# Performance work log

Measured on AMD Instinct MI355X. Metric: run time of the kernel, lower is better.

The kernel has to match this reference:

```python
import jax, jax.numpy as jnp
import numpy as np

NUM_CLASSES = 20
N_IN = 1024      # input_capsule_num
C_IN = 128       # in_channels
C_OUT = 64       # out_channels
NUM_ITERS = 3


def squash(x, axis):
    # squash_v1: scale = sqrt(|s|^2) / (0.5 + |s|^2)
    s2 = jnp.sum(x * x, axis=axis, keepdims=True)
    scale = jnp.sqrt(s2) / (0.5 + s2)
    return scale * x


def setup_inputs() -> dict:
    key = jax.random.key(0)
    kx, kw = jax.random.split(key)
    x = jax.random.normal(kx, (32, N_IN, C_IN), dtype=jnp.float32)
    # xavier_uniform over the torch [1, N, C, out, in] tensor: fan_in = in, fan_out = out
    limit = float(np.sqrt(6.0 / (C_IN + C_OUT)))
    w1 = jax.random.uniform(kw, (N_IN, NUM_CLASSES, C_OUT, C_IN), dtype=jnp.float32,
                            minval=-limit, maxval=limit)
    return {"x": x, "w1": w1}


def reference(x, w1):
    # u_hat[b,n,c,d] = w1[n,c,d,i] @ x[b,n,i]  (torch.matmul of [B,N,C,out,in] @ [B,N,C,in,1])
    u_hat = jnp.einsum('ncdi,bni->bncd', w1, x)  # [B, N, C, D]
    B = x.shape[0]
    b_ij = jnp.zeros((B, N_IN, NUM_CLASSES), dtype=u_hat.dtype)
    u_hat_sq = squash(u_hat, axis=3)  # squash over out-channel dim (loop-invariant)
    v = None
    for i in range(NUM_ITERS):
        c = jax.nn.softmax(b_ij, axis=2)                 # softmax over classes
        c = c / jnp.sum(c, axis=1, keepdims=True)        # normalize over input capsules
        s = jnp.einsum('bnc,bncd->bcd', c, u_hat)        # weighted sum over n
        v = squash(s, axis=2)                            # [B, C, D]
        if i < NUM_ITERS - 1:
            dd = 1.0 - jnp.sum((u_hat_sq - v[:, None]) ** 2, axis=3)  # [B, N, C]
            b_ij = b_ij + dd
    poses = v[..., None]                                  # [B, C, D, 1]
    activations = jnp.sqrt(jnp.sum(poses ** 2, axis=2))   # [B, C, 1]
    return poses, activations
```

## Files before the change

kernel.cpp:

```cpp
#include <hip/hip_runtime.h>
#include <hip/hip_bf16.h>


#define NCLS 20
#define NIN  1024
#define CIN  128
#define DOUT 64
#define BATCH 32
#define MCD  1280

typedef __attribute__((ext_vector_type(8))) short bf16x8;
typedef __attribute__((ext_vector_type(4))) float f32x4;

__device__ __forceinline__ float b2f(unsigned short u) {
    union { unsigned int i; float f; } v; v.i = ((unsigned int)u) << 16; return v.f;
}
__device__ __forceinline__ unsigned short f2b_rne(float f) {
    union { float f; unsigned int i; } v; v.f = f;
    unsigned int x = v.i;
    return (unsigned short)((x + 0x7fffu + ((x >> 16) & 1u)) >> 16);
}
__device__ __forceinline__ void cvt_hilo(const float* v, bf16x8& h, bf16x8& l) {
#pragma unroll
    for (int j = 0; j < 8; ++j) {
        unsigned short hb = f2b_rne(v[j]);
        h[j] = (short)hb;
        l[j] = (short)f2b_rne(v[j] - b2f(hb));
    }
}

__global__ __launch_bounds__(256) void pass_uhat(
    const float* __restrict__ x, const float* __restrict__ W,
    unsigned short* __restrict__ uhat)
{
    const int n    = blockIdx.x >> 1;
    const int half = blockIdx.x & 1;
    const int t    = threadIdx.x;
    const int wave = t >> 6;
    const int lane = t & 63;
    const int lm   = lane & 15;
    const int lq   = lane >> 4;

    bf16x8 xh[2][4], xl[2][4];
#pragma unroll
    for (int mt = 0; mt < 2; ++mt) {
        const float* xrow = x + ((size_t)(mt * 16 + lm) * NIN + n) * CIN + lq * 8;
#pragma unroll
        for (int ks = 0; ks < 4; ++ks) {
            float v[8];
            *reinterpret_cast<float4*>(&v[0]) = *reinterpret_cast<const float4*>(xrow + ks * 32);
            *reinterpret_cast<float4*>(&v[4]) = *reinterpret_cast<const float4*>(xrow + ks * 32 + 4);
            cvt_hilo(v, xh[mt][ks], xl[mt][ks]);
        }
    }

    const int nt0 = half * 40 + wave * 10;
    for (int ntc = 0; ntc < 10; ++ntc) {
        const int nt = nt0 + ntc;
        const float* wp = W + ((size_t)n * MCD + nt * 16 + lm) * CIN + lq * 8;
        f32x4 acc0 = {0.f, 0.f, 0.f, 0.f};
        f32x4 acc1 = {0.f, 0.f, 0.f, 0.f};
#pragma unroll
        for (int ks = 0; ks < 4; ++ks) {
            float v[8];
            *reinterpret_cast<float4*>(&v[0]) = *reinterpret_cast<const float4*>(wp + ks * 32);
            *reinterpret_cast<float4*>(&v[4]) = *reinterpret_cast<const float4*>(wp + ks * 32 + 4);
            bf16x8 wh, wl;
            cvt_hilo(v, wh, wl);
            acc0 = __builtin_amdgcn_mfma_f32_16x16x32_bf16(xh[0][ks], wh, acc0, 0, 0, 0);
            acc1 = __builtin_amdgcn_mfma_f32_16x16x32_bf16(xh[1][ks], wh, acc1, 0, 0, 0);
            acc0 = __builtin_amdgcn_mfma_f32_16x16x32_bf16(xh[0][ks], wl, acc0, 0, 0, 0);
            acc1 = __builtin_amdgcn_mfma_f32_16x16x32_bf16(xh[1][ks], wl, acc1, 0, 0, 0);
            acc0 = __builtin_amdgcn_mfma_f32_16x16x32_bf16(xl[0][ks], wh, acc0, 0, 0, 0);
            acc1 = __builtin_amdgcn_mfma_f32_16x16x32_bf16(xl[1][ks], wh, acc1, 0, 0, 0);
        }
        const int cd = nt * 16 + lm;
#pragma unroll
        for (int mt = 0; mt < 2; ++mt) {
            f32x4 a = mt ? acc1 : acc0;
#pragma unroll
            for (int r = 0; r < 4; ++r) {
                int br = mt * 16 + lq * 4 + r;
                uhat[((size_t)br * NIN + n) * MCD + cd] = f2b_rne(a[r]);
            }
        }
    }
}

__global__ __launch_bounds__(320) void pass_s0(
    const unsigned short* __restrict__ uhat, float* __restrict__ s0raw)
{
    const int b     = blockIdx.x >> 4;
    const int chunk = blockIdx.x & 15;
    const int t     = threadIdx.x;

    const ushort4* base = reinterpret_cast<const ushort4*>(
        uhat + ((size_t)b * NIN + chunk * 64) * MCD) + t;
    float a0 = 0.f, a1 = 0.f, a2 = 0.f, a3 = 0.f;
#pragma unroll 4
    for (int k = 0; k < 64; ++k) {
        ushort4 u = base[(size_t)k * 320];
        a0 += b2f(u.x); a1 += b2f(u.y); a2 += b2f(u.z); a3 += b2f(u.w);
    }
    float* dst = s0raw + (size_t)b * MCD + t * 4;
    atomicAdd(dst + 0, a0);
    atomicAdd(dst + 1, a1);
    atomicAdd(dst + 2, a2);
    atomicAdd(dst + 3, a3);
}

__global__ void pass_v(const float* __restrict__ sraw, const float* __restrict__ Zc,
                       float invz_uniform, float* __restrict__ vbuf,
                       float* __restrict__ vn2,
                       float* __restrict__ out_poses, float* __restrict__ out_act)
{
    const int bc   = blockIdx.x;
    const int lane = threadIdx.x;
    const int idx  = bc * 64 + lane;
    float inv = (Zc != nullptr) ? (1.0f / Zc[bc]) : invz_uniform;
    float s  = sraw[idx] * inv;
    float s2 = s * s;
#pragma unroll
    for (int o = 32; o >= 1; o >>= 1) s2 += __shfl_xor(s2, o, 64);
    float norm  = sqrtf(s2);
    float scale = norm / (0.5f + s2);
    float v = scale * s;
    vbuf[idx] = v;
    float vn = scale * scale * s2;
    if (lane == 0) vn2[bc] = vn;
    if (out_poses != nullptr) {
        out_poses[idx] = v;
        if (lane == 0) out_act[bc] = sqrtf(vn);
    }
}

__global__ __launch_bounds__(256) void pass_route(
    const unsigned short* __restrict__ uhat, const float* __restrict__ vbuf,
    const float* __restrict__ vn2, float* __restrict__ bij,
    float* __restrict__ snext, float* __restrict__ Znext)
{
    const int b     = blockIdx.x >> 5;
    const int chunk = blockIdx.x & 31;
    const int t     = threadIdx.x;
    const int wave  = t >> 6;
    const int lane  = t & 63;

    __shared__ float Vs[20 * 65];
    __shared__ float sred[4][20 * 65];
    __shared__ float qrow[4][20], prow[4][20], scrow[4][20], zred[4][20];

    for (int idx = t; idx < 20 * 65; idx += 256) {
        int cc = idx / 65, dd = idx % 65;
        Vs[idx] = (dd < 64) ? vbuf[(size_t)b * MCD + cc * 64 + dd] : 0.f;
    }
    __syncthreads();

    const int cmy   = lane >> 4;
    const int dbase = (lane & 15) * 4;
    const float vnb = vn2[b * NCLS + (lane < 20 ? lane : 0)];

    float sacc[5][4];
#pragma unroll
    for (int tt = 0; tt < 5; ++tt)
#pragma unroll
        for (int j = 0; j < 4; ++j) sacc[tt][j] = 0.f;
    float zacc = 0.f;

    for (int k = 0; k < 8; ++k) {
        const int n = chunk * 32 + wave * 8 + k;
        const ushort4* up = reinterpret_cast<const ushort4*>(
            uhat + ((size_t)b * NIN + n) * MCD);

        float uf[5][4];
#pragma unroll
        for (int tt = 0; tt < 5; ++tt) {
            ushort4 uq = up[tt * 64 + lane];
            uf[tt][0] = b2f(uq.x); uf[tt][1] = b2f(uq.y);
            uf[tt][2] = b2f(uq.z); uf[tt][3] = b2f(uq.w);
        }
#pragma unroll
        for (int tt = 0; tt < 5; ++tt) {
            int cc = tt * 4 + cmy;
            float q = 0.f, p = 0.f;
#pragma unroll
            for (int j = 0; j < 4; ++j) {
                float u = uf[tt][j];
                q = fmaf(u, u, q);
                p = fmaf(u, Vs[cc * 65 + dbase + j], p);
            }
#pragma unroll
            for (int o = 8; o >= 1; o >>= 1) {
                q += __shfl_xor(q, o, 16);
                p += __shfl_xor(p, o, 16);
            }
            if ((lane & 15) == 0) { qrow[wave][cc] = q; prow[wave][cc] = p; }
        }
        {
            float val = -1e30f;
            if (lane < 20) {
                float q  = qrow[wave][lane];
                float p  = prow[wave][lane];
                float qs = sqrtf(q);
                float su = qs / (0.5f + q);
                float dd = 1.f - su * su * q + 2.f * su * p - vnb;
                size_t bidx = ((size_t)b * NIN + n) * NCLS + lane;
                float bnew = bij[bidx] + dd;
                bij[bidx] = bnew;
                val = bnew;
            }
            float mx = val;
#pragma unroll
            for (int o = 16; o >= 1; o >>= 1) mx = fmaxf(mx, __shfl_xor(mx, o, 32));
            float e = (lane < 20) ? __expf(val - mx) : 0.f;
            float se = e;
#pragma unroll
            for (int o = 16; o >= 1; o >>= 1) se += __shfl_xor(se, o, 32);
            if (lane < 20) {
                float sc = e / se;
                scrow[wave][lane] = sc;
                zacc += sc;
            }
        }
#pragma unroll
        for (int tt = 0; tt < 5; ++tt) {
            float sc = scrow[wave][tt * 4 + cmy];
#pragma unroll
            for (int j = 0; j < 4; ++j)
                sacc[tt][j] = fmaf(sc, uf[tt][j], sacc[tt][j]);
        }
    }

#pragma unroll
    for (int tt = 0; tt < 5; ++tt) {
        int cc = tt * 4 + cmy;
#pragma unroll
        for (int j = 0; j < 4; ++j)
            sred[wave][cc * 65 + dbase + j] = sacc[tt][j];
    }
    if (lane < 20) zred[wave][lane] = zacc;
    __syncthreads();

    for (int idx = t; idx < NCLS * DOUT; idx += 256) {
        int cc = idx >> 6, dd = idx & 63;
        int a  = cc * 65 + dd;
        float sum = sred[0][a] + sred[1][a] + sred[2][a] + sred[3][a];
        atomicAdd(&snext[(size_t)(b * NCLS + cc) * DOUT + dd], sum);
    }
    if (t < 20) {
        float z = zred[0][t] + zred[1][t] + zred[2][t] + zred[3][t];
        atomicAdd(&Znext[b * NCLS + t], z);
    }
}

extern "C" void kernel_launch(void* const* d_in, const int* in_sizes, int n_in,
                              void* d_out, int out_size, void* d_ws, size_t ws_size,
                              hipStream_t stream)
{
    (void)in_sizes; (void)n_in; (void)out_size; (void)ws_size;
    const float* x  = (const float*)d_in[0];
    const float* w1 = (const float*)d_in[1];
    float* out = (float*)d_out;

    char* ws = (char*)d_ws;
    unsigned short* uhat = (unsigned short*)ws;
    size_t off = (size_t)BATCH * NIN * MCD * 2;
    float* s0   = (float*)(ws + off); off += (size_t)BATCH * MCD * 4;
    float* s1   = (float*)(ws + off); off += (size_t)BATCH * MCD * 4;
    float* s2   = (float*)(ws + off); off += (size_t)BATCH * MCD * 4;
    float* Z1   = (float*)(ws + off); off += (size_t)BATCH * NCLS * 4;
    float* Z2   = (float*)(ws + off); off += (size_t)BATCH * NCLS * 4;
    float* bij  = (float*)(ws + off); off += (size_t)BATCH * NIN * NCLS * 4;
    float* vbuf = (float*)(ws + off); off += (size_t)BATCH * MCD * 4;
    float* vn2  = (float*)(ws + off); off += (size_t)BATCH * NCLS * 4;

    size_t zbytes = (size_t)3 * BATCH * MCD * 4 + 2 * BATCH * NCLS * 4
                  + (size_t)BATCH * NIN * NCLS * 4;
    hipMemsetAsync(s0, 0, zbytes, stream);

    pass_uhat <<<NIN * 2, 256, 0, stream>>>(x, w1, uhat);
    pass_s0   <<<BATCH * 16, 320, 0, stream>>>(uhat, s0);
    pass_v    <<<BATCH * NCLS, 64, 0, stream>>>(s0, nullptr, 1.0f / 1024.0f,
                                                vbuf, vn2, nullptr, nullptr);
    pass_route<<<BATCH * 32, 256, 0, stream>>>(uhat, vbuf, vn2, bij, s1, Z1);
    pass_v    <<<BATCH * NCLS, 64, 0, stream>>>(s1, Z1, 0.f, vbuf, vn2, nullptr, nullptr);
    pass_route<<<BATCH * 32, 256, 0, stream>>>(uhat, vbuf, vn2, bij, s2, Z2);
    pass_v    <<<BATCH * NCLS, 64, 0, stream>>>(s2, Z2, 0.f, vbuf, vn2,
                                                out, out + BATCH * MCD);
}
```

Baseline: 1.012 ms.

## Double-buffer weight loads in uhat GEMM and split routing across more blocks

The uhat kernel now prefetches the next weight tile into a second register buffer while the current tile is converted and fed to MFMA. This software pipeline is meant to hide global load latency, at the cost of more live registers. The routing kernel doubles its grid so each wave handles 4 input capsules instead of 8, and its fully unrolled loop double-buffers the per-wave LDS rows. It also replaces the per-wave LDS reduction with LDS atomics into a single shared accumulator. The finer split raises parallelism but doubles the global atomic traffic to snext and Z.

After: 1.127 ms. +11.4%, slower.

```diff
diff --git a/kernel.cpp b/kernel.cpp
--- a/kernel.cpp
+++ b/kernel.cpp
@@ -55,36 +55,55 @@
     }
 
     const int nt0 = half * 40 + wave * 10;
-    for (int ntc = 0; ntc < 10; ++ntc) {
-        const int nt = nt0 + ntc;
-        const float* wp = W + ((size_t)n * MCD + nt * 16 + lm) * CIN + lq * 8;
-        f32x4 acc0 = {0.f, 0.f, 0.f, 0.f};
-        f32x4 acc1 = {0.f, 0.f, 0.f, 0.f};
-#pragma unroll
-        for (int ks = 0; ks < 4; ++ks) {
-            float v[8];
-            *reinterpret_cast<float4*>(&v[0]) = *reinterpret_cast<const float4*>(wp + ks * 32);
-            *reinterpret_cast<float4*>(&v[4]) = *reinterpret_cast<const float4*>(wp + ks * 32 + 4);
-            bf16x8 wh, wl;
-            cvt_hilo(v, wh, wl);
-            acc0 = __builtin_amdgcn_mfma_f32_16x16x32_bf16(xh[0][ks], wh, acc0, 0, 0, 0);
-            acc1 = __builtin_amdgcn_mfma_f32_16x16x32_bf16(xh[1][ks], wh, acc1, 0, 0, 0);
-            acc0 = __builtin_amdgcn_mfma_f32_16x16x32_bf16(xh[0][ks], wl, acc0, 0, 0, 0);
-            acc1 = __builtin_amdgcn_mfma_f32_16x16x32_bf16(xh[1][ks], wl, acc1, 0, 0, 0);
-            acc0 = __builtin_amdgcn_mfma_f32_16x16x32_bf16(xl[0][ks], wh, acc0, 0, 0, 0);
-            acc1 = __builtin_amdgcn_mfma_f32_16x16x32_bf16(xl[1][ks], wh, acc1, 0, 0, 0);
-        }
-        const int cd = nt * 16 + lm;
-#pragma unroll
-        for (int mt = 0; mt < 2; ++mt) {
-            f32x4 a = mt ? acc1 : acc0;
-#pragma unroll
-            for (int r = 0; r < 4; ++r) {
-                int br = mt * 16 + lq * 4 + r;
-                uhat[((size_t)br * NIN + n) * MCD + cd] = f2b_rne(a[r]);
-            }
-        }
-    }
+    const float* wbase = W + (size_t)n * MCD * CIN;
+
+    float4 wA[8], wB[8];
+
+#define ISSUE(NTC, BUF) do {                                                   \
+    const float* wp_ = wbase + (size_t)((nt0 + (NTC)) * 16 + lm) * CIN + lq*8; \
+    _Pragma("unroll")                                                          \
+    for (int ks = 0; ks < 4; ++ks) {                                           \
+        BUF[2*ks]   = *reinterpret_cast<const float4*>(wp_ + ks * 32);         \
+        BUF[2*ks+1] = *reinterpret_cast<const float4*>(wp_ + ks * 32 + 4);     \
+    } } while (0)
+
+#define COMPUTE(NTC, BUF) do {                                                 \
+    f32x4 acc0 = {0.f,0.f,0.f,0.f};                                            \
+    f32x4 acc1 = {0.f,0.f,0.f,0.f};                                            \
+    _Pragma("unroll")                                                          \
+    for (int ks = 0; ks < 4; ++ks) {                                           \
+        float v_[8];                                                           \
+        *reinterpret_cast<float4*>(&v_[0]) = BUF[2*ks];                        \
+        *reinterpret_cast<float4*>(&v_[4]) = BUF[2*ks+1];                      \
+        bf16x8 wh_, wl_;                                                       \
+        cvt_hilo(v_, wh_, wl_);                                                \
+        acc0 = __builtin_amdgcn_mfma_f32_16x16x32_bf16(xh[0][ks], wh_, acc0, 0,0,0); \
+        acc1 = __builtin_amdgcn_mfma_f32_16x16x32_bf16(xh[1][ks], wh_, acc1, 0,0,0); \
+        acc0 = __builtin_amdgcn_mfma_f32_16x16x32_bf16(xh[0][ks], wl_, acc0, 0,0,0); \
+        acc1 = __builtin_amdgcn_mfma_f32_16x16x32_bf16(xh[1][ks], wl_, acc1, 0,0,0); \
+        acc0 = __builtin_amdgcn_mfma_f32_16x16x32_bf16(xl[0][ks], wh_, acc0, 0,0,0); \
+        acc1 = __builtin_amdgcn_mfma_f32_16x16x32_bf16(xl[1][ks], wh_, acc1, 0,0,0); \
+    }                                                                          \
+    const int cd_ = (nt0 + (NTC)) * 16 + lm;                                   \
+    _Pragma("unroll")                                                          \
+    for (int mt = 0; mt < 2; ++mt) {                                           \
+        f32x4 a_ = mt ? acc1 : acc0;                                           \
+        _Pragma("unroll")                                                      \
+        for (int r = 0; r < 4; ++r) {                                          \
+            int br_ = mt * 16 + lq * 4 + r;                                    \
+            uhat[((size_t)br_ * NIN + n) * MCD + cd_] = f2b_rne(a_[r]);        \
+        } } } while (0)
+
+    ISSUE(0, wA);
+#pragma unroll
+    for (int p = 0; p < 5; ++p) {
+        ISSUE(2*p + 1, wB);
+        COMPUTE(2*p, wA);
+        if (p < 4) ISSUE(2*p + 2, wA);
+        COMPUTE(2*p + 1, wB);
+    }
+#undef ISSUE
+#undef COMPUTE
 }
 
 __global__ __launch_bounds__(320) void pass_s0(
@@ -139,20 +158,23 @@
     const float* __restrict__ vn2, float* __restrict__ bij,
     float* __restrict__ snext, float* __restrict__ Znext)
 {
-    const int b     = blockIdx.x >> 5;
-    const int chunk = blockIdx.x & 31;
+    const int b     = blockIdx.x >> 6;
+    const int chunk = blockIdx.x & 63;
     const int t     = threadIdx.x;
     const int wave  = t >> 6;
     const int lane  = t & 63;
 
     __shared__ float Vs[20 * 65];
-    __shared__ float sred[4][20 * 65];
-    __shared__ float qrow[4][20], prow[4][20], scrow[4][20], zred[4][20];
+    __shared__ float sacc_sh[20 * 64];
+    __shared__ float zsh[20];
+    __shared__ float qrow[4][2][20], prow[4][2][20], scrow[4][2][20];
 
     for (int idx = t; idx < 20 * 65; idx += 256) {
         int cc = idx / 65, dd = idx % 65;
         Vs[idx] = (dd < 64) ? vbuf[(size_t)b * MCD + cc * 64 + dd] : 0.f;
     }
+    for (int idx = t; idx < 20 * 64; idx += 256) sacc_sh[idx] = 0.f;
+    if (t < 20) zsh[t] = 0.f;
     __syncthreads();
 
     const int cmy   = lane >> 4;
@@ -166,8 +188,11 @@
         for (int j = 0; j < 4; ++j) sacc[tt][j] = 0.f;
     float zacc = 0.f;
 
-    for (int k = 0; k < 8; ++k) {
-        const int n = chunk * 32 + wave * 8 + k;
+    const int n0 = chunk * 16 + wave * 4;
+#pragma unroll
+    for (int k = 0; k < 4; ++k) {
+        const int n   = n0 + k;
+        const int par = k & 1;
         const ushort4* up = reinterpret_cast<const ushort4*>(
             uhat + ((size_t)b * NIN + n) * MCD);
 
@@ -193,13 +218,13 @@
                 q += __shfl_xor(q, o, 16);
                 p += __shfl_xor(p, o, 16);
             }
-            if ((lane & 15) == 0) { qrow[wave][cc] = q; prow[wave][cc] = p; }
+            if ((lane & 15) == 0) { qrow[wave][par][cc] = q; prow[wave][par][cc] = p; }
         }
         {
             float val = -1e30f;
             if (lane < 20) {
-                float q  = qrow[wave][lane];
-                float p  = prow[wave][lane];
+                float q  = qrow[wave][par][lane];
+                float p  = prow[wave][par][lane];
                 float qs = sqrtf(q);
                 float su = qs / (0.5f + q);
                 float dd = 1.f - su * su * q + 2.f * su * p - vnb;
@@ -217,13 +242,13 @@
             for (int o = 16; o >= 1; o >>= 1) se += __shfl_xor(se, o, 32);
             if (lane < 20) {
                 float sc = e / se;
-                scrow[wave][lane] = sc;
+                scrow[wave][par][lane] = sc;
                 zacc += sc;
             }
         }
 #pragma unroll
         for (int tt = 0; tt < 5; ++tt) {
-            float sc = scrow[wave][tt * 4 + cmy];
+            float sc = scrow[wave][par][tt * 4 + cmy];
 #pragma unroll
             for (int j = 0; j < 4; ++j)
                 sacc[tt][j] = fmaf(sc, uf[tt][j], sacc[tt][j]);
@@ -235,21 +260,16 @@
         int cc = tt * 4 + cmy;
 #pragma unroll
         for (int j = 0; j < 4; ++j)
-            sred[wave][cc * 65 + dbase + j] = sacc[tt][j];
-    }
-    if (lane < 20) zred[wave][lane] = zacc;
+            atomicAdd(&sacc_sh[cc * 64 + dbase + j], sacc[tt][j]);
+    }
+    if (lane < 20) atomicAdd(&zsh[lane], zacc);
     __syncthreads();
 
     for (int idx = t; idx < NCLS * DOUT; idx += 256) {
         int cc = idx >> 6, dd = idx & 63;
-        int a  = cc * 65 + dd;
-        float sum = sred[0][a] + sred[1][a] + sred[2][a] + sred[3][a];
-        atomicAdd(&snext[(size_t)(b * NCLS + cc) * DOUT + dd], sum);
-    }
-    if (t < 20) {
-        float z = zred[0][t] + zred[1][t] + zred[2][t] + zred[3][t];
-        atomicAdd(&Znext[b * NCLS + t], z);
-    }
+        atomicAdd(&snext[(size_t)(b * NCLS + cc) * DOUT + dd], sacc_sh[idx]);
+    }
+    if (t < 20) atomicAdd(&Znext[b * NCLS + t], zsh[t]);
 }
 
 extern "C" void kernel_launch(void* const* d_in, const int* in_sizes, int n_in,
@@ -281,9 +301,9 @@
     pass_s0   <<<BATCH * 16, 320, 0, stream>>>(uhat, s0);
     pass_v    <<<BATCH * NCLS, 64, 0, stream>>>(s0, nullptr, 1.0f / 1024.0f,
                                                 vbuf, vn2, nullptr, nullptr);
-    pass_route<<<BATCH * 32, 256, 0, stream>>>(uhat, vbuf, vn2, bij, s1, Z1);
+    pass_route<<<BATCH * 64, 256, 0, stream>>>(uhat, vbuf, vn2, bij, s1, Z1);
     pass_v    <<<BATCH * NCLS, 64, 0, stream>>>(s1, Z1, 0.f, vbuf, vn2, nullptr, nullptr);
-    pass_route<<<BATCH * 32, 256, 0, stream>>>(uhat, vbuf, vn2, bij, s2, Z2);
+    pass_route<<<BATCH * 64, 256, 0, stream>>>(uhat, vbuf, vn2, bij, s2, Z2);
     pass_v    <<<BATCH * NCLS, 64, 0, stream>>>(s2, Z2, 0.f, vbuf, vn2,
                                                 out, out + BATCH * MCD);
 }
```
